# Performance work log

Measured on AMD Instinct MI355X. Metric: run time of the kernel, lower is better.

The kernel has to match this reference:

```python
import jax, jax.numpy as jnp
import numpy as np

MASK_INFTY_APPROX = 1e30
B, L, D = 2, 2048, 1024
H = 16
HD = D // H  # 64
NCODE = 512


def setup_inputs() -> dict:
    key = jax.random.key(0)
    ks = jax.random.split(key, 6)
    s = 1.0 / np.sqrt(D)
    x = jax.random.normal(ks[0], (B, L, D), dtype=jnp.float32)
    Wq = jax.random.normal(ks[1], (D, D), dtype=jnp.float32) * s
    Wk = jax.random.normal(ks[2], (D, D), dtype=jnp.float32) * s
    Wv = jax.random.normal(ks[3], (D, D), dtype=jnp.float32) * s
    Wo = jax.random.normal(ks[4], (D, D), dtype=jnp.float32) * s
    codebook = jax.random.normal(ks[5], (H, NCODE, HD), dtype=jnp.float32)
    return {"x": x, "Wq": Wq, "Wk": Wk, "Wv": Wv, "Wo": Wo, "codebook": codebook}


def _vq(k, codebook):
    # k: [B,H,L,hd], codebook: [H,C,hd]
    dot = jnp.einsum('bhld,hcd->bhlc', k, codebook)
    k2 = jnp.sum(k * k, axis=-1, keepdims=True)            # [B,H,L,1]
    c2 = jnp.sum(codebook * codebook, axis=-1)             # [H,C]
    d2 = k2 - 2.0 * dot + c2[None, :, None, :]             # [B,H,L,C]
    shortcodes = jnp.argmin(d2, axis=-1)                   # [B,H,L]
    h_idx = jnp.arange(H)[None, :, None]
    c_sel = codebook[h_idx, shortcodes]                    # [B,H,L,hd]
    # straight-through quantization
    k_hat = k + jax.lax.stop_gradient(c_sel - k)
    l_commit = jnp.mean(jnp.sum((k - jax.lax.stop_gradient(c_sel)) ** 2, axis=-1))
    l_codebook = jnp.mean(jnp.sum((jax.lax.stop_gradient(k) - c_sel) ** 2, axis=-1))
    return k_hat, shortcodes, l_commit, l_codebook


def reference(x, Wq, Wk, Wv, Wo, codebook):
    q = jnp.einsum('bld,de->ble', x, Wq.T).reshape(B, L, H, HD).transpose(0, 2, 1, 3)
    k = jnp.einsum('bld,de->ble', x, Wk.T).reshape(B, L, H, HD).transpose(0, 2, 1, 3)
    v = jnp.einsum('bld,de->ble', x, Wv.T).reshape(B, L, H, HD).transpose(0, 2, 1, 3)
    k_hat, shortcodes, l_commit, l_codebook = _vq(k, codebook)
    scale = HD ** (-0.5)
    logits = jnp.einsum('bhld,bhtd->bhlt', q, k_hat) * scale  # [B,H,L,L]
    causal_mask = jnp.tril(jnp.ones((L, L), dtype=bool))
    logits = jnp.where(causal_mask[None, None], logits, -MASK_INFTY_APPROX)
    w = jax.nn.softmax(logits, axis=-1)
    attn = jnp.einsum('bhlt,bhtd->bhld', w, v)
    attn = attn.transpose(0, 2, 1, 3).reshape(B, L, D)
    out = jnp.einsum('bld,de->ble', attn, Wo.T)
    return out, l_commit, l_codebook, shortcodes
```

## Files before the change

kernel.cpp:

```cpp
#include <hip/hip_runtime.h>
#include <stdint.h>

#define BB 2
#define HH 16
#define LL 2048
#define DD 1024
#define HDD 64
#define NC 512

typedef __bf16 bf16x8 __attribute__((ext_vector_type(8)));
typedef float f32x4 __attribute__((ext_vector_type(4)));
typedef unsigned short u16x8 __attribute__((ext_vector_type(8)));
typedef unsigned short u16x4 __attribute__((ext_vector_type(4)));

__device__ __forceinline__ unsigned short f2bf(float f) {
  union { float f; unsigned u; } v; v.f = f;
  unsigned u = v.u;
  u += 0x7fffu + ((u >> 16) & 1u);
  return (unsigned short)(u >> 16);
}
__device__ __forceinline__ float bf2f(unsigned short h) {
  union { unsigned u; float f; } v; v.u = ((unsigned)h) << 16;
  return v.f;
}

__device__ __forceinline__ void load_lds16(const unsigned short* g, unsigned short* l) {
  __builtin_amdgcn_global_load_lds((const __attribute__((address_space(1))) void*)g,
                                   (__attribute__((address_space(3))) void*)l, 16, 0, 0);
}

__global__ void cast_all(const float* __restrict__ x, const float* __restrict__ wq,
                         const float* __restrict__ wk, const float* __restrict__ wv,
                         const float* __restrict__ wo, const float* __restrict__ cb,
                         unsigned short* __restrict__ xb, unsigned short* __restrict__ xl,
                         unsigned short* __restrict__ wb, unsigned short* __restrict__ wkl,
                         unsigned short* __restrict__ wob, unsigned short* __restrict__ cbb,
                         unsigned short* __restrict__ cbl, float* __restrict__ lsum) {
  long i = (long)blockIdx.x * blockDim.x + threadIdx.x;
  if (i == 0) lsum[0] = 0.f;
  const long NX4 = 1048576, NW4 = 262144, NCB4 = 131072;
  const long TOT4 = NX4 + 4 * NW4 + NCB4;
  for (long q = i; q < TOT4; q += (long)gridDim.x * blockDim.x) {
    if (q < NX4) {
      long t = q * 4;
      float4 v = *(const float4*)(x + t);
      u16x4 hi, lo;
#pragma unroll
      for (int j = 0; j < 4; j++) {
        float f = ((const float*)&v)[j];
        unsigned short h = f2bf(f);
        hi[j] = h; lo[j] = f2bf(f - bf2f(h));
      }
      *(u16x4*)(xb + t) = hi;
      *(u16x4*)(xl + t) = lo;
    } else if (q < NX4 + NW4) {
      long t = (q - NX4) * 4;
      float4 v = *(const float4*)(wq + t);
      u16x4 hi;
#pragma unroll
      for (int j = 0; j < 4; j++) hi[j] = f2bf(((const float*)&v)[j]);
      *(u16x4*)(wb + t) = hi;
    } else if (q < NX4 + 2 * NW4) {
      long t = (q - NX4 - NW4) * 4;
      float4 v = *(const float4*)(wk + t);
      u16x4 hi, lo;
#pragma unroll
      for (int j = 0; j < 4; j++) {
        float f = ((const float*)&v)[j];
        unsigned short h = f2bf(f);
        hi[j] = h; lo[j] = f2bf(f - bf2f(h));
      }
      *(u16x4*)(wb + 1048576 + t) = hi;
      *(u16x4*)(wkl + t) = lo;
    } else if (q < NX4 + 3 * NW4) {
      long t = (q - NX4 - 2 * NW4) * 4;
      float4 v = *(const float4*)(wv + t);
      u16x4 hi;
#pragma unroll
      for (int j = 0; j < 4; j++) hi[j] = f2bf(((const float*)&v)[j]);
      *(u16x4*)(wb + 2097152 + t) = hi;
    } else if (q < NX4 + 4 * NW4) {
      long t = (q - NX4 - 3 * NW4) * 4;
      float4 v = *(const float4*)(wo + t);
      u16x4 hi;
#pragma unroll
      for (int j = 0; j < 4; j++) hi[j] = f2bf(((const float*)&v)[j]);
      *(u16x4*)(wob + t) = hi;
    } else {
      long t = (q - NX4 - 4 * NW4) * 4;
      float4 v = *(const float4*)(cb + t);
      u16x4 hi, lo;
#pragma unroll
      for (int j = 0; j < 4; j++) {
        float f = ((const float*)&v)[j];
        unsigned short h = f2bf(f);
        hi[j] = h; lo[j] = f2bf(f - bf2f(h));
      }
      *(u16x4*)(cbb + t) = hi;
      *(u16x4*)(cbl + t) = lo;
    }
  }
}

__global__ void c2_kernel(const float* __restrict__ cb, float* __restrict__ c2) {
  int i = blockIdx.x * blockDim.x + threadIdx.x;
  if (i >= HH * NC) return;
  const float* r = cb + (long)i * HDD;
  double s = 0.0;
  for (int j = 0; j < HDD; j++) s += (double)r[j] * (double)r[j];
  c2[i] = (float)s;
}

__global__ __launch_bounds__(256) void gemm_qv(
    const unsigned short* __restrict__ xb, const unsigned short* __restrict__ wb,
    unsigned short* __restrict__ qb, unsigned short* __restrict__ vt) {
  __shared__ __align__(16) unsigned short As[128 * 32];
  __shared__ __align__(16) unsigned short Bs[128 * 32];
  int tid = threadIdx.x;
  int wave = tid >> 6, lane = tid & 63;
  int quad = lane >> 4, col = lane & 15;
  int m0 = blockIdx.y * 128;
  int n0 = blockIdx.x * 128 + (blockIdx.x >= 8 ? 1024 : 0);
  f32x4 acc[4][4] = {};
  int row_in = (wave << 4) + (lane >> 2);
  int seg = lane & 3;
  const unsigned short* gA0 = xb + (long)(m0 + row_in) * DD + seg * 8;
  const unsigned short* gA1 = xb + (long)(m0 + 64 + row_in) * DD + seg * 8;
  const unsigned short* gB0 = wb + (long)(n0 + row_in) * DD + seg * 8;
  const unsigned short* gB1 = wb + (long)(n0 + 64 + row_in) * DD + seg * 8;
  unsigned short* lA0 = As + wave * 512;
  unsigned short* lA1 = As + 2048 + wave * 512;
  unsigned short* lB0 = Bs + wave * 512;
  unsigned short* lB1 = Bs + 2048 + wave * 512;
  int wm = wave & 1, wn = wave >> 1;
  const unsigned short* pa = As + (wm * 64 + col) * 32 + quad * 8;
  const unsigned short* pb = Bs + (wn * 64 + col) * 32 + quad * 8;
  for (int kk = 0; kk < DD; kk += 32) {
    __syncthreads();
    load_lds16(gA0 + kk, lA0);
    load_lds16(gA1 + kk, lA1);
    load_lds16(gB0 + kk, lB0);
    load_lds16(gB1 + kk, lB1);
    __syncthreads();
    bf16x8 af[4], bfr[4];
    for (int t = 0; t < 4; t++) af[t]  = *(const bf16x8*)(pa + t * 512);
    for (int t = 0; t < 4; t++) bfr[t] = *(const bf16x8*)(pb + t * 512);
    for (int mt = 0; mt < 4; mt++)
      for (int nt = 0; nt < 4; nt++)
        acc[mt][nt] = __builtin_amdgcn_mfma_f32_16x16x32_bf16(af[mt], bfr[nt], acc[mt][nt], 0, 0, 0);
  }
  for (int mt = 0; mt < 4; mt++)
    for (int nt = 0; nt < 4; nt++) {
      int mbase = m0 + wm * 64 + mt * 16 + quad * 4;
      int n = n0 + wn * 64 + nt * 16 + col;
      int which = n >> 10, e = n & 1023;
      int h = e >> 6, hd = e & 63;
      for (int r = 0; r < 4; r++) {
        int m = mbase + r;
        int b = m >> 11, l = m & 2047;
        unsigned short val = f2bf(acc[mt][nt][r]);
        long bh = (long)(b * HH + h);
        if (which == 0)      qb[(bh * LL + l) * HDD + hd] = val;
        else                 vt[(bh * HDD + hd) * LL + l] = val;
      }
    }
}

__global__ __launch_bounds__(256) void kvq(
    const unsigned short* __restrict__ xb, const unsigned short* __restrict__ xl,
    const unsigned short* __restrict__ wb, const unsigned short* __restrict__ wkl,
    const float* __restrict__ cb, const float* __restrict__ c2,
    const unsigned short* __restrict__ cbb, const unsigned short* __restrict__ cbl,
    unsigned short* __restrict__ khat, float* __restrict__ scodes,
    float* __restrict__ lsum) {
  __shared__ __align__(16) char smem[53248];
  unsigned short* Ah = (unsigned short*)smem;
  unsigned short* Al = (unsigned short*)(smem + 8192);
  unsigned short* Bh = (unsigned short*)(smem + 16384);
  unsigned short* Bl = (unsigned short*)(smem + 20480);
  float* kfL = (float*)smem;
  unsigned short* CbHb = (unsigned short*)(smem + 34816);
  unsigned short* CbLb = (unsigned short*)(smem + 44032);

  int tid = threadIdx.x;
  int wave = tid >> 6, lane = tid & 63;
  int quad = lane >> 4, col = lane & 15;
  int id = blockIdx.y * 16 + blockIdx.x;
  int xcd = id & 7, sidx = id >> 3;
  int mt4 = xcd * 4 + (sidx >> 4);
  int h = sidx & 15;
  int m0 = mt4 * 128;
  int n0 = h * 64;
  int bgl = m0 >> 11;
  int l0 = m0 & 2047;
  long bh = (long)(bgl * HH + h);
  const float* c2h = c2 + h * NC;

  f32x4 acc[4][2] = {};
  int row_in = (wave << 4) + (lane >> 2);
  int seg = lane & 3;
  const unsigned short* gAh0 = xb + (long)(m0 + row_in) * DD + seg * 8;
  const unsigned short* gAh1 = xb + (long)(m0 + 64 + row_in) * DD + seg * 8;
  const unsigned short* gAl0 = xl + (long)(m0 + row_in) * DD + seg * 8;
  const unsigned short* gAl1 = xl + (long)(m0 + 64 + row_in) * DD + seg * 8;
  const unsigned short* gBh  = wb + (long)(1048576 + (long)(n0 + row_in) * DD) + seg * 8;
  const unsigned short* gBl  = wkl + (long)(n0 + row_in) * DD + seg * 8;
  unsigned short* lAh0 = Ah + wave * 512;
  unsigned short* lAh1 = Ah + 2048 + wave * 512;
  unsigned short* lAl0 = Al + wave * 512;
  unsigned short* lAl1 = Al + 2048 + wave * 512;
  unsigned short* lBh  = Bh + wave * 512;
  unsigned short* lBl  = Bl + wave * 512;
  int wm = wave & 1, wn = wave >> 1;
  const unsigned short* pah = Ah + (wm * 64 + col) * 32 + quad * 8;
  const unsigned short* pal = Al + (wm * 64 + col) * 32 + quad * 8;
  const unsigned short* pbh = Bh + (wn * 32 + col) * 32 + quad * 8;
  const unsigned short* pbl = Bl + (wn * 32 + col) * 32 + quad * 8;
  for (int kk = 0; kk < DD; kk += 32) {
    __syncthreads();
    load_lds16(gAh0 + kk, lAh0);
    load_lds16(gAh1 + kk, lAh1);
    load_lds16(gAl0 + kk, lAl0);
    load_lds16(gAl1 + kk, lAl1);
    load_lds16(gBh + kk, lBh);
    load_lds16(gBl + kk, lBl);
    __syncthreads();
    bf16x8 ah[4], al[4], bhf[2], blf[2];
    for (int t = 0; t < 4; t++) ah[t] = *(const bf16x8*)(pah + t * 512);
    for (int t = 0; t < 4; t++) al[t] = *(const bf16x8*)(pal + t * 512);
    for (int t = 0; t < 2; t++) bhf[t] = *(const bf16x8*)(pbh + t * 512);
    for (int t = 0; t < 2; t++) blf[t] = *(const bf16x8*)(pbl + t * 512);
    for (int mt = 0; mt < 4; mt++)
      for (int nt = 0; nt < 2; nt++) {
        acc[mt][nt] = __builtin_amdgcn_mfma_f32_16x16x32_bf16(ah[mt], bhf[nt], acc[mt][nt], 0, 0, 0);
        acc[mt][nt] = __builtin_amdgcn_mfma_f32_16x16x32_bf16(ah[mt], blf[nt], acc[mt][nt], 0, 0, 0);
        acc[mt][nt] = __builtin_amdgcn_mfma_f32_16x16x32_bf16(al[mt], bhf[nt], acc[mt][nt], 0, 0, 0);
      }
  }
  __syncthreads();
  const unsigned short* cbbh = cbb + (long)h * NC * HDD;
  const unsigned short* cblh = cbl + (long)h * NC * HDD;
  int srow = tid >> 3;
  int sseg = (tid & 7) * 8;
  const unsigned short* gH = cbbh + (long)srow * HDD + sseg;
  const unsigned short* gL = cblh + (long)srow * HDD + sseg;
  int ldsOff = srow * 72 + sseg;
  u16x8 ph0 = *(const u16x8*)(gH);
  u16x8 pl0 = *(const u16x8*)(gL);
  for (int mt = 0; mt < 4; mt++)
    for (int nt = 0; nt < 2; nt++) {
      int rbasew = wm * 64 + mt * 16 + quad * 4;
      int hd = wn * 32 + nt * 16 + col;
      for (int r = 0; r < 4; r++)
        kfL[(rbasew + r) * 68 + hd] = acc[mt][nt][r];
    }
  *(u16x8*)(CbHb + ldsOff) = ph0;
  *(u16x8*)(CbLb + ldsOff) = pl0;
  __syncthreads();

  bf16x8 bfh[2][2], bfl[2][2];
  float k2g[2];
#pragma unroll
  for (int g = 0; g < 2; g++) {
    const float* kp = kfL + (wave * 32 + g * 16 + col) * 68 + quad * 8;
    float4 t0 = *(const float4*)(kp);
    float4 t1 = *(const float4*)(kp + 4);
    float4 t2 = *(const float4*)(kp + 32);
    float4 t3 = *(const float4*)(kp + 36);
    float fv[16];
    fv[0]=t0.x; fv[1]=t0.y; fv[2]=t0.z; fv[3]=t0.w;
    fv[4]=t1.x; fv[5]=t1.y; fv[6]=t1.z; fv[7]=t1.w;
    fv[8]=t2.x; fv[9]=t2.y; fv[10]=t2.z; fv[11]=t2.w;
    fv[12]=t3.x; fv[13]=t3.y; fv[14]=t3.z; fv[15]=t3.w;
    float k2 = 0.f;
#pragma unroll
    for (int j = 0; j < 16; j++) k2 = fmaf(fv[j], fv[j], k2);
    k2 += __shfl_xor(k2, 16);
    k2 += __shfl_xor(k2, 32);
    k2g[g] = k2;
    u16x8 h0, h1, l0u, l1u;
#pragma unroll
    for (int j = 0; j < 8; j++) {
      unsigned short hi = f2bf(fv[j]);
      h0[j] = hi; l0u[j] = f2bf(fv[j] - bf2f(hi));
      unsigned short hi2 = f2bf(fv[8 + j]);
      h1[j] = hi2; l1u[j] = f2bf(fv[8 + j] - bf2f(hi2));
    }
    bfh[g][0] = __builtin_bit_cast(bf16x8, h0);
    bfh[g][1] = __builtin_bit_cast(bf16x8, h1);
    bfl[g][0] = __builtin_bit_cast(bf16x8, l0u);
    bfl[g][1] = __builtin_bit_cast(bf16x8, l1u);
  }
  float b1v[2] = {1e38f, 1e38f}, b2v[2] = {1e38f, 1e38f};
  int b1i[2] = {0x7fffffff, 0x7fffffff}, b2i[2] = {0x7fffffff, 0x7fffffff};
  for (int t = 0; t < 16; t++) {
    int cur = t & 1;
    u16x8 nh, nl;
    if (t < 15) {
      nh = *(const u16x8*)(gH + (t + 1) * 32 * HDD);
      nl = *(const u16x8*)(gL + (t + 1) * 32 * HDD);
    }
    const unsigned short* CbHc = CbHb + cur * 2304;
    const unsigned short* CbLc = CbLb + cur * 2304;
#pragma unroll
    for (int s = 0; s < 2; s++) {
      const unsigned short* rp = CbHc + (s * 16 + col) * 72 + quad * 8;
      const unsigned short* rq = CbLc + (s * 16 + col) * 72 + quad * 8;
      bf16x8 ah0 = *(const bf16x8*)(rp);
      bf16x8 ah1 = *(const bf16x8*)(rp + 32);
      bf16x8 al0 = *(const bf16x8*)(rq);
      bf16x8 al1 = *(const bf16x8*)(rq + 32);
      f32x4 aP0 = {}, aQ0 = {}, aP1 = {}, aQ1 = {};
      aP0 = __builtin_amdgcn_mfma_f32_16x16x32_bf16(ah0, bfh[0][0], aP0, 0, 0, 0);
      aQ0 = __builtin_amdgcn_mfma_f32_16x16x32_bf16(ah1, bfh[0][1], aQ0, 0, 0, 0);
      aP1 = __builtin_amdgcn_mfma_f32_16x16x32_bf16(ah0, bfh[1][0], aP1, 0, 0, 0);
      aQ1 = __builtin_amdgcn_mfma_f32_16x16x32_bf16(ah1, bfh[1][1], aQ1, 0, 0, 0);
      aP0 = __builtin_amdgcn_mfma_f32_16x16x32_bf16(al0, bfh[0][0], aP0, 0, 0, 0);
      aQ0 = __builtin_amdgcn_mfma_f32_16x16x32_bf16(al1, bfh[0][1], aQ0, 0, 0, 0);
      aP1 = __builtin_amdgcn_mfma_f32_16x16x32_bf16(al0, bfh[1][0], aP1, 0, 0, 0);
      aQ1 = __builtin_amdgcn_mfma_f32_16x16x32_bf16(al1, bfh[1][1], aQ1, 0, 0, 0);
      aP0 = __builtin_amdgcn_mfma_f32_16x16x32_bf16(ah0, bfl[0][0], aP0, 0, 0, 0);
      aQ0 = __builtin_amdgcn_mfma_f32_16x16x32_bf16(ah1, bfl[0][1], aQ0, 0, 0, 0);
      aP1 = __builtin_amdgcn_mfma_f32_16x16x32_bf16(ah0, bfl[1][0], aP1, 0, 0, 0);
      aQ1 = __builtin_amdgcn_mfma_f32_16x16x32_bf16(ah1, bfl[1][1], aQ1, 0, 0, 0);
      f32x4 c2v = *(const f32x4*)(c2h + t * 32 + s * 16 + quad * 4);
#pragma unroll
      for (int r = 0; r < 4; r++) {
        int idx = t * 32 + s * 16 + quad * 4 + r;
        float v0 = c2v[r] - 2.0f * (aP0[r] + aQ0[r]);
        if (v0 < b1v[0]) { b2v[0] = b1v[0]; b2i[0] = b1i[0]; b1v[0] = v0; b1i[0] = idx; }
        else if (v0 < b2v[0]) { b2v[0] = v0; b2i[0] = idx; }
        float v1 = c2v[r] - 2.0f * (aP1[r] + aQ1[r]);
        if (v1 < b1v[1]) { b2v[1] = b1v[1]; b2i[1] = b1i[1]; b1v[1] = v1; b1i[1] = idx; }
        else if (v1 < b2v[1]) { b2v[1] = v1; b2i[1] = idx; }
      }
    }
    if (t < 15) {
      *(u16x8*)(CbHb + (cur ^ 1) * 2304 + ldsOff) = nh;
      *(u16x8*)(CbLb + (cur ^ 1) * 2304 + ldsOff) = nl;
    }
    __syncthreads();
  }
  const float DMARG = 0.015625f;
  float partT = 0.f;
  int w0 = 0, w1 = 0;
#pragma unroll
  for (int g = 0; g < 2; g++) {
    float v1 = b1v[g], v2 = b2v[g];
    int i1 = b1i[g], i2 = b2i[g];
#pragma unroll
    for (int d = 16; d <= 32; d <<= 1) {
      float o1v = __shfl_xor(v1, d); int o1i = __shfl_xor(i1, d);
      float o2v = __shfl_xor(v2, d); int o2i = __shfl_xor(i2, d);
      if (o1v < v1 || (o1v == v1 && o1i < i1)) {
        float nv; int ni;
        if (v1 < o2v || (v1 == o2v && i1 < o2i)) { nv = v1; ni = i1; }
        else { nv = o2v; ni = o2i; }
        v1 = o1v; i1 = o1i; v2 = nv; i2 = ni;
      } else {
        if (o1v < v2 || (o1v == v2 && o1i < i2)) { v2 = o1v; i2 = o1i; }
      }
    }
    bool trig = (v2 - v1 <= DMARG);
    float part;
    int widx = i1;
    if (__any(trig)) {
      const float* kpr = kfL + (wave * 32 + g * 16 + col) * 68 + quad * 8;
      float4 f0 = *(const float4*)(kpr);
      float4 f1 = *(const float4*)(kpr + 4);
      float4 f2 = *(const float4*)(kpr + 32);
      float4 f3 = *(const float4*)(kpr + 36);
      const float* c1p = cb + ((long)h * NC + i1) * HDD + quad * 8;
      const float* c2p = cb + ((long)h * NC + i2) * HDD + quad * 8;
      float4 a0 = *(const float4*)(c1p);
      float4 a1 = *(const float4*)(c1p + 4);
      float4 a2 = *(const float4*)(c1p + 32);
      float4 a3 = *(const float4*)(c1p + 36);
      float4 e0 = *(const float4*)(c2p);
      float4 e1 = *(const float4*)(c2p + 4);
      float4 e2 = *(const float4*)(c2p + 32);
      float4 e3 = *(const float4*)(c2p + 36);
      float s1 = 0.f, s2 = 0.f;
#pragma unroll
      for (int j = 0; j < 4; j++) {
        float d;
        d = ((const float*)&f0)[j] - ((const float*)&a0)[j]; s1 = fmaf(d, d, s1);
        d = ((const float*)&f1)[j] - ((const float*)&a1)[j]; s1 = fmaf(d, d, s1);
        d = ((const float*)&f2)[j] - ((const float*)&a2)[j]; s1 = fmaf(d, d, s1);
        d = ((const float*)&f3)[j] - ((const float*)&a3)[j]; s1 = fmaf(d, d, s1);
        d = ((const float*)&f0)[j] - ((const float*)&e0)[j]; s2 = fmaf(d, d, s2);
        d = ((const float*)&f1)[j] - ((const float*)&e1)[j]; s2 = fmaf(d, d, s2);
        d = ((const float*)&f2)[j] - ((const float*)&e2)[j]; s2 = fmaf(d, d, s2);
        d = ((const float*)&f3)[j] - ((const float*)&e3)[j]; s2 = fmaf(d, d, s2);
      }
      s1 += __shfl_xor(s1, 16); s1 += __shfl_xor(s1, 32);
      s2 += __shfl_xor(s2, 16); s2 += __shfl_xor(s2, 32);
      if (trig) {
        if (s2 < s1 || (s2 == s1 && i2 < i1)) { widx = i2; part = s2; }
        else { widx = i1; part = s1; }
      } else {
        part = k2g[g] + v1;
      }
    } else {
      part = k2g[g] + v1;
    }
    if (g == 0) w0 = widx; else w1 = widx;
    if (quad == 0) partT += part;
    if (lane < 16)
      scodes[bh * LL + l0 + wave * 32 + g * 16 + lane] = (float)widx;
  }
  partT += __shfl_xor(partT, 1);  partT += __shfl_xor(partT, 2);
  partT += __shfl_xor(partT, 4);  partT += __shfl_xor(partT, 8);
  partT += __shfl_xor(partT, 16); partT += __shfl_xor(partT, 32);
  if (lane == 0) atomicAdd(lsum, partT);
  {
    int rL = lane >> 1;
    int srcl = rL & 15;
    int c0 = __shfl(w0, srcl);
    int c1 = __shfl(w1, srcl);
    int code = (rL >> 4) ? c1 : c0;
    int p = (lane & 1) * 32;
    const unsigned short* src = cbbh + (long)code * HDD + p;
    unsigned short* dst = khat + (bh * LL + l0 + wave * 32 + rL) * HDD + p;
    *(u16x8*)(dst)      = *(const u16x8*)(src);
    *(u16x8*)(dst + 8)  = *(const u16x8*)(src + 8);
    *(u16x8*)(dst + 16) = *(const u16x8*)(src + 16);
    *(u16x8*)(dst + 24) = *(const u16x8*)(src + 24);
  }
}

__global__ __launch_bounds__(256) void attn_kernel(
    const unsigned short* __restrict__ qb, const unsigned short* __restrict__ khat,
    const unsigned short* __restrict__ vt, unsigned short* __restrict__ attnb) {
  __shared__ __align__(16) unsigned short Pbuf[4][2][16 * 72];
  __shared__ __align__(16) unsigned short Kbuf[64 * 72];
  __shared__ __align__(16) unsigned short Vbuf[64 * 72];
  int tid = threadIdx.x, wave = tid >> 6, lane = tid & 63;
  int quad = lane >> 4, col = lane & 15;
  int id = blockIdx.y * 16 + blockIdx.x;
  int xcd = id & 7, sidx = id >> 3;
  int bh = xcd * 4 + (sidx >> 4);
  int pi = sidx & 15;
  int b = bh >> 4, h = bh & 15;
  int ta = pi, tb = 31 - pi;
  int qbA = ta * 64 + wave * 16;
  int qbB = tb * 64 + wave * 16;
  const unsigned short* qrA = qb + ((long)bh * LL + qbA + col) * HDD;
  const unsigned short* qrB = qb + ((long)bh * LL + qbB + col) * HDD;
  bf16x8 aqA0 = *(const bf16x8*)(qrA + quad * 8);
  bf16x8 aqA1 = *(const bf16x8*)(qrA + 32 + quad * 8);
  bf16x8 aqB0 = *(const bf16x8*)(qrB + quad * 8);
  bf16x8 aqB1 = *(const bf16x8*)(qrB + 32 + quad * 8);
  float lA = 0.f, lB = 0.f;
  f32x4 oA[4] = {}, oB[4] = {};
  unsigned short* PA = Pbuf[wave][0];
  unsigned short* PB = Pbuf[wave][1];
  const unsigned short* kh = khat + (long)bh * LL * HDD;
  const unsigned short* vh = vt + (long)bh * HDD * LL;
  int srow = tid >> 2, sc = (tid & 3) * 8;
  const unsigned short* gK = kh + (long)srow * HDD + sc;
// ... 74 lines not shown
    for (int nt = 0; nt < 4; nt++) {
      const unsigned short* vrow = Vbuf + (nt * 16 + col) * 72;
      bf16x8 v0 = *(const bf16x8*)(vrow + quad * 8);
      bf16x8 v1 = *(const bf16x8*)(vrow + 32 + quad * 8);
      oB[nt] = __builtin_amdgcn_mfma_f32_16x16x32_bf16(apB0, v0, oB[nt], 0, 0, 0);
      oB[nt] = __builtin_amdgcn_mfma_f32_16x16x32_bf16(apB1, v1, oB[nt], 0, 0, 0);
      if (actA) {
        oA[nt] = __builtin_amdgcn_mfma_f32_16x16x32_bf16(apA0, v0, oA[nt], 0, 0, 0);
        oA[nt] = __builtin_amdgcn_mfma_f32_16x16x32_bf16(apA1, v1, oA[nt], 0, 0, 0);
      }
    }
  }
  lA += __shfl_xor(lA, 16); lA += __shfl_xor(lA, 32);
  lB += __shfl_xor(lB, 16); lB += __shfl_xor(lB, 32);
  float invAc = 1.0f / lA;
  float invBc = 1.0f / lB;
  for (int r = 0; r < 4; r++) {
    float invA = __shfl(invAc, quad * 4 + r);
    float invB = __shfl(invBc, quad * 4 + r);
    int rowA = qbA + quad * 4 + r;
    int rowB = qbB + quad * 4 + r;
    for (int nt = 0; nt < 4; nt++) {
      int hd = nt * 16 + col;
      attnb[((long)b * LL + rowA) * DD + h * HDD + hd] = f2bf(oA[nt][r] * invA);
      attnb[((long)b * LL + rowB) * DD + h * HDD + hd] = f2bf(oB[nt][r] * invB);
    }
  }
}

__global__ __launch_bounds__(256) void gemm_out(
    const unsigned short* __restrict__ attnb, const unsigned short* __restrict__ wob,
    float* __restrict__ out) {
  __shared__ __align__(16) unsigned short As[128 * 32];
  __shared__ __align__(16) unsigned short Bs[128 * 32];
  int tid = threadIdx.x;
  int wave = tid >> 6, lane = tid & 63;
  int quad = lane >> 4, col = lane & 15;
  int m0 = blockIdx.y * 128;
  int n0 = blockIdx.x * 128;
  f32x4 acc[4][4] = {};
  int row_in = (wave << 4) + (lane >> 2);
  int seg = lane & 3;
  const unsigned short* gA0 = attnb + (long)(m0 + row_in) * DD + seg * 8;
  const unsigned short* gA1 = attnb + (long)(m0 + 64 + row_in) * DD + seg * 8;
  const unsigned short* gB0 = wob + (long)(n0 + row_in) * DD + seg * 8;
  const unsigned short* gB1 = wob + (long)(n0 + 64 + row_in) * DD + seg * 8;
  unsigned short* lA0 = As + wave * 512;
  unsigned short* lA1 = As + 2048 + wave * 512;
  unsigned short* lB0 = Bs + wave * 512;
  unsigned short* lB1 = Bs + 2048 + wave * 512;
  int wm = wave & 1, wn = wave >> 1;
  const unsigned short* pa = As + (wm * 64 + col) * 32 + quad * 8;
  const unsigned short* pb = Bs + (wn * 64 + col) * 32 + quad * 8;
  for (int kk = 0; kk < DD; kk += 32) {
    __syncthreads();
    load_lds16(gA0 + kk, lA0);
    load_lds16(gA1 + kk, lA1);
    load_lds16(gB0 + kk, lB0);
    load_lds16(gB1 + kk, lB1);
    __syncthreads();
    bf16x8 af[4], bfr[4];
    for (int t = 0; t < 4; t++) af[t]  = *(const bf16x8*)(pa + t * 512);
    for (int t = 0; t < 4; t++) bfr[t] = *(const bf16x8*)(pb + t * 512);
    for (int mt = 0; mt < 4; mt++)
      for (int nt = 0; nt < 4; nt++)
        acc[mt][nt] = __builtin_amdgcn_mfma_f32_16x16x32_bf16(af[mt], bfr[nt], acc[mt][nt], 0, 0, 0);
  }
  for (int mt = 0; mt < 4; mt++)
    for (int nt = 0; nt < 4; nt++) {
      int mbase = m0 + wm * 64 + mt * 16 + quad * 4;
      int n = n0 + wn * 64 + nt * 16 + col;
      for (int r = 0; r < 4; r++)
        out[(long)(mbase + r) * DD + n] = acc[mt][nt][r];
    }
}

__global__ void finalize(const float* __restrict__ lsum, float* __restrict__ out) {
  if (threadIdx.x == 0) {
    float v = lsum[0] / (float)(BB * HH * LL);
    out[4194304] = v;
    out[4194305] = v;
  }
}

extern "C" void kernel_launch(void* const* d_in, const int* in_sizes, int n_in,
                              void* d_out, int out_size, void* d_ws, size_t ws_size,
                              hipStream_t stream) {
  const float* x  = (const float*)d_in[0];
  const float* wq = (const float*)d_in[1];
  const float* wk = (const float*)d_in[2];
  const float* wv = (const float*)d_in[3];
  const float* wo = (const float*)d_in[4];
  const float* cb = (const float*)d_in[5];
  float* out = (float*)d_out;

  char* ws = (char*)d_ws;
  size_t off = 0;
  auto alloc = [&](size_t bytes) {
    void* p = ws + off;
    off = (off + bytes + 255) & ~(size_t)255;
    return p;
  };
  unsigned short* xb    = (unsigned short*)alloc(4194304 * 2);
  unsigned short* xl    = (unsigned short*)alloc(4194304 * 2);
  unsigned short* wb    = (unsigned short*)alloc(3145728 * 2);
  unsigned short* wkl   = (unsigned short*)alloc(1048576 * 2);
  unsigned short* wob   = (unsigned short*)alloc(1048576 * 2);
  unsigned short* cbb   = (unsigned short*)alloc(524288 * 2);
  unsigned short* cbl   = (unsigned short*)alloc(524288 * 2);
  unsigned short* qb    = (unsigned short*)alloc(4194304 * 2);
  unsigned short* vt    = (unsigned short*)alloc(4194304 * 2);
  unsigned short* khat  = (unsigned short*)alloc(4194304 * 2);
  unsigned short* attnb = (unsigned short*)alloc(4194304 * 2);
  float* c2   = (float*)alloc(8192 * 4);
  float* lsum = (float*)alloc(256);

  cast_all<<<dim3(4096), dim3(256), 0, stream>>>(x, wq, wk, wv, wo, cb, xb, xl, wb, wkl, wob, cbb, cbl, lsum);
  c2_kernel<<<dim3(32), dim3(256), 0, stream>>>(cb, c2);
  gemm_qv<<<dim3(16, 32), dim3(256), 0, stream>>>(xb, wb, qb, vt);
  kvq<<<dim3(16, 32), dim3(256), 0, stream>>>(xb, xl, wb, wkl, cb, c2, cbb, cbl, khat, out + 4194306, lsum);
  attn_kernel<<<dim3(16, 32), dim3(256), 0, stream>>>(qb, khat, vt, attnb);
  gemm_out<<<dim3(8, 32), dim3(256), 0, stream>>>(attnb, wob, out);
  finalize<<<dim3(1), dim3(64), 0, stream>>>(lsum, out);
}
```

Measured before the change: 290.6 us.

## Merge QV GEMM and K-VQ into one interleaved launch with smaller tiles

Folds the codebook-norm computation into the cast kernel and merges the Q/V projection GEMM and the K projection plus VQ kernel into one launch. Block indices are interleaved so the two jobs run side by side. The K/VQ tile shrinks from 128 to 64 rows, giving more blocks, and the codebook norms are staged in LDS. The output GEMM N-tile is halved to 64 so it launches twice as many blocks. This cuts launch count and tail idle time and raises occupancy, at the cost of less per-block reuse and possibly uneven block runtimes within the merged grid.

```diff
diff --git a/kernel.cpp b/kernel.cpp
--- a/kernel.cpp
+++ b/kernel.cpp
@@ -35,12 +35,23 @@
                          unsigned short* __restrict__ xb, unsigned short* __restrict__ xl,
                          unsigned short* __restrict__ wb, unsigned short* __restrict__ wkl,
                          unsigned short* __restrict__ wob, unsigned short* __restrict__ cbb,
-                         unsigned short* __restrict__ cbl, float* __restrict__ lsum) {
+                         unsigned short* __restrict__ cbl, float* __restrict__ c2,
+                         float* __restrict__ lsum) {
+  if (blockIdx.x >= 4096) {
+    int i = (blockIdx.x - 4096) * 256 + threadIdx.x;
+    if (i < HH * NC) {
+      const float* r = cb + (long)i * HDD;
+      double s = 0.0;
+      for (int j = 0; j < HDD; j++) s += (double)r[j] * (double)r[j];
+      c2[i] = (float)s;
+    }
+    return;
+  }
   long i = (long)blockIdx.x * blockDim.x + threadIdx.x;
   if (i == 0) lsum[0] = 0.f;
   const long NX4 = 1048576, NW4 = 262144, NCB4 = 131072;
   const long TOT4 = NX4 + 4 * NW4 + NCB4;
-  for (long q = i; q < TOT4; q += (long)gridDim.x * blockDim.x) {
+  for (long q = i; q < TOT4; q += (long)4096 * blockDim.x) {
     if (q < NX4) {
       long t = q * 4;
       float4 v = *(const float4*)(x + t);
@@ -102,135 +113,124 @@
   }
 }
 
-__global__ void c2_kernel(const float* __restrict__ cb, float* __restrict__ c2) {
-  int i = blockIdx.x * blockDim.x + threadIdx.x;
-  if (i >= HH * NC) return;
-  const float* r = cb + (long)i * HDD;
-  double s = 0.0;
-  for (int j = 0; j < HDD; j++) s += (double)r[j] * (double)r[j];
-  c2[i] = (float)s;
-}
-
-__global__ __launch_bounds__(256) void gemm_qv(
-    const unsigned short* __restrict__ xb, const unsigned short* __restrict__ wb,
-    unsigned short* __restrict__ qb, unsigned short* __restrict__ vt) {
-  __shared__ __align__(16) unsigned short As[128 * 32];
-  __shared__ __align__(16) unsigned short Bs[128 * 32];
-  int tid = threadIdx.x;
-  int wave = tid >> 6, lane = tid & 63;
-  int quad = lane >> 4, col = lane & 15;
-  int m0 = blockIdx.y * 128;
-  int n0 = blockIdx.x * 128 + (blockIdx.x >= 8 ? 1024 : 0);
-  f32x4 acc[4][4] = {};
-  int row_in = (wave << 4) + (lane >> 2);
-  int seg = lane & 3;
-  const unsigned short* gA0 = xb + (long)(m0 + row_in) * DD + seg * 8;
-  const unsigned short* gA1 = xb + (long)(m0 + 64 + row_in) * DD + seg * 8;
-  const unsigned short* gB0 = wb + (long)(n0 + row_in) * DD + seg * 8;
-  const unsigned short* gB1 = wb + (long)(n0 + 64 + row_in) * DD + seg * 8;
-  unsigned short* lA0 = As + wave * 512;
-  unsigned short* lA1 = As + 2048 + wave * 512;
-  unsigned short* lB0 = Bs + wave * 512;
-  unsigned short* lB1 = Bs + 2048 + wave * 512;
-  int wm = wave & 1, wn = wave >> 1;
-  const unsigned short* pa = As + (wm * 64 + col) * 32 + quad * 8;
-  const unsigned short* pb = Bs + (wn * 64 + col) * 32 + quad * 8;
-  for (int kk = 0; kk < DD; kk += 32) {
-    __syncthreads();
-    load_lds16(gA0 + kk, lA0);
-    load_lds16(gA1 + kk, lA1);
-    load_lds16(gB0 + kk, lB0);
-    load_lds16(gB1 + kk, lB1);
-    __syncthreads();
-    bf16x8 af[4], bfr[4];
-    for (int t = 0; t < 4; t++) af[t]  = *(const bf16x8*)(pa + t * 512);
-    for (int t = 0; t < 4; t++) bfr[t] = *(const bf16x8*)(pb + t * 512);
-    for (int mt = 0; mt < 4; mt++)
-      for (int nt = 0; nt < 4; nt++)
-        acc[mt][nt] = __builtin_amdgcn_mfma_f32_16x16x32_bf16(af[mt], bfr[nt], acc[mt][nt], 0, 0, 0);
-  }
-  for (int mt = 0; mt < 4; mt++)
-    for (int nt = 0; nt < 4; nt++) {
-      int mbase = m0 + wm * 64 + mt * 16 + quad * 4;
-      int n = n0 + wn * 64 + nt * 16 + col;
-      int which = n >> 10, e = n & 1023;
-      int h = e >> 6, hd = e & 63;
-      for (int r = 0; r < 4; r++) {
-        int m = mbase + r;
-        int b = m >> 11, l = m & 2047;
-        unsigned short val = f2bf(acc[mt][nt][r]);
-        long bh = (long)(b * HH + h);
-        if (which == 0)      qb[(bh * LL + l) * HDD + hd] = val;
-        else                 vt[(bh * HDD + hd) * LL + l] = val;
-      }
-    }
-}
-
-__global__ __launch_bounds__(256) void kvq(
+__global__ __launch_bounds__(256) void qv_kvq(
     const unsigned short* __restrict__ xb, const unsigned short* __restrict__ xl,
     const unsigned short* __restrict__ wb, const unsigned short* __restrict__ wkl,
     const float* __restrict__ cb, const float* __restrict__ c2,
     const unsigned short* __restrict__ cbb, const unsigned short* __restrict__ cbl,
+    unsigned short* __restrict__ qb, unsigned short* __restrict__ vt,
     unsigned short* __restrict__ khat, float* __restrict__ scodes,
     float* __restrict__ lsum) {
-  __shared__ __align__(16) char smem[53248];
-  unsigned short* Ah = (unsigned short*)smem;
-  unsigned short* Al = (unsigned short*)(smem + 8192);
-  unsigned short* Bh = (unsigned short*)(smem + 16384);
-  unsigned short* Bl = (unsigned short*)(smem + 20480);
-  float* kfL = (float*)smem;
-  unsigned short* CbHb = (unsigned short*)(smem + 34816);
-  unsigned short* CbLb = (unsigned short*)(smem + 44032);
-
+  __shared__ __align__(16) char smem[37888];
   int tid = threadIdx.x;
   int wave = tid >> 6, lane = tid & 63;
   int quad = lane >> 4, col = lane & 15;
-  int id = blockIdx.y * 16 + blockIdx.x;
-  int xcd = id & 7, sidx = id >> 3;
-  int mt4 = xcd * 4 + (sidx >> 4);
-  int h = sidx & 15;
-  int m0 = mt4 * 128;
+  int gid = blockIdx.x;
+  int cls = gid % 3;
+
+  if (cls == 2) {
+    unsigned short* As = (unsigned short*)smem;
+    unsigned short* Bs = (unsigned short*)(smem + 8192);
+    int qid = gid / 3;
+    int bx = qid & 15, by = qid >> 4;
+    int m0 = by * 128;
+    int n0 = bx * 128 + (bx >= 8 ? 1024 : 0);
+    f32x4 acc[4][4] = {};
+    int row_in = (wave << 4) + (lane >> 2);
+    int seg = lane & 3;
+    const unsigned short* gA0 = xb + (long)(m0 + row_in) * DD + seg * 8;
+    const unsigned short* gA1 = xb + (long)(m0 + 64 + row_in) * DD + seg * 8;
+    const unsigned short* gB0 = wb + (long)(n0 + row_in) * DD + seg * 8;
+    const unsigned short* gB1 = wb + (long)(n0 + 64 + row_in) * DD + seg * 8;
+    unsigned short* lA0 = As + wave * 512;
+    unsigned short* lA1 = As + 2048 + wave * 512;
+    unsigned short* lB0 = Bs + wave * 512;
+    unsigned short* lB1 = Bs + 2048 + wave * 512;
+    int wm = wave & 1, wn = wave >> 1;
+    const unsigned short* pa = As + (wm * 64 + col) * 32 + quad * 8;
+    const unsigned short* pb = Bs + (wn * 64 + col) * 32 + quad * 8;
+    for (int kk = 0; kk < DD; kk += 32) {
+      __syncthreads();
+      load_lds16(gA0 + kk, lA0);
+      load_lds16(gA1 + kk, lA1);
+      load_lds16(gB0 + kk, lB0);
+      load_lds16(gB1 + kk, lB1);
+      __syncthreads();
+      bf16x8 af[4], bfr[4];
+      for (int t = 0; t < 4; t++) af[t]  = *(const bf16x8*)(pa + t * 512);
+      for (int t = 0; t < 4; t++) bfr[t] = *(const bf16x8*)(pb + t * 512);
+      for (int mt = 0; mt < 4; mt++)
+        for (int nt = 0; nt < 4; nt++)
+          acc[mt][nt] = __builtin_amdgcn_mfma_f32_16x16x32_bf16(af[mt], bfr[nt], acc[mt][nt], 0, 0, 0);
+    }
+    for (int mt = 0; mt < 4; mt++)
+      for (int nt = 0; nt < 4; nt++) {
+        int mbase = m0 + wm * 64 + mt * 16 + quad * 4;
+        int n = n0 + wn * 64 + nt * 16 + col;
+        int which = n >> 10, e = n & 1023;
+        int h = e >> 6, hd = e & 63;
+        for (int r = 0; r < 4; r++) {
+          int m = mbase + r;
+          int b = m >> 11, l = m & 2047;
+          unsigned short val = f2bf(acc[mt][nt][r]);
+          long bh = (long)(b * HH + h);
+          if (which == 0)      qb[(bh * LL + l) * HDD + hd] = val;
+          else                 vt[(bh * HDD + hd) * LL + l] = val;
+        }
+      }
+    return;
+  }
+
+  unsigned short* Ah = (unsigned short*)smem;
+  unsigned short* Al = (unsigned short*)(smem + 4096);
+  unsigned short* Bh = (unsigned short*)(smem + 8192);
+  unsigned short* Bl = (unsigned short*)(smem + 12288);
+  float* kfL = (float*)smem;
+  unsigned short* CbHb = (unsigned short*)(smem + 17408);
+  unsigned short* CbLb = (unsigned short*)(smem + 26624);
+  float* Cs = (float*)(smem + 35840);
+
+  int kid = (gid / 3) * 2 + cls;
+  int mtile = kid & 63;
+  int h = kid >> 6;
+  int m0 = mtile * 64;
   int n0 = h * 64;
   int bgl = m0 >> 11;
   int l0 = m0 & 2047;
   long bh = (long)(bgl * HH + h);
   const float* c2h = c2 + h * NC;
-
-  f32x4 acc[4][2] = {};
+  Cs[tid] = c2h[tid];
+  Cs[tid + 256] = c2h[tid + 256];
+
+  f32x4 acc[2][2] = {};
   int row_in = (wave << 4) + (lane >> 2);
   int seg = lane & 3;
-  const unsigned short* gAh0 = xb + (long)(m0 + row_in) * DD + seg * 8;
-  const unsigned short* gAh1 = xb + (long)(m0 + 64 + row_in) * DD + seg * 8;
-  const unsigned short* gAl0 = xl + (long)(m0 + row_in) * DD + seg * 8;
-  const unsigned short* gAl1 = xl + (long)(m0 + 64 + row_in) * DD + seg * 8;
-  const unsigned short* gBh  = wb + (long)(1048576 + (long)(n0 + row_in) * DD) + seg * 8;
-  const unsigned short* gBl  = wkl + (long)(n0 + row_in) * DD + seg * 8;
-  unsigned short* lAh0 = Ah + wave * 512;
-  unsigned short* lAh1 = Ah + 2048 + wave * 512;
-  unsigned short* lAl0 = Al + wave * 512;
-  unsigned short* lAl1 = Al + 2048 + wave * 512;
-  unsigned short* lBh  = Bh + wave * 512;
-  unsigned short* lBl  = Bl + wave * 512;
+  const unsigned short* gAh = xb + (long)(m0 + row_in) * DD + seg * 8;
+  const unsigned short* gAl = xl + (long)(m0 + row_in) * DD + seg * 8;
+  const unsigned short* gBh = wb + (long)(1048576 + (long)(n0 + row_in) * DD) + seg * 8;
+  const unsigned short* gBl = wkl + (long)(n0 + row_in) * DD + seg * 8;
+  unsigned short* lAh = Ah + wave * 512;
+  unsigned short* lAl = Al + wave * 512;
+  unsigned short* lBh = Bh + wave * 512;
+  unsigned short* lBl = Bl + wave * 512;
   int wm = wave & 1, wn = wave >> 1;
-  const unsigned short* pah = Ah + (wm * 64 + col) * 32 + quad * 8;
-  const unsigned short* pal = Al + (wm * 64 + col) * 32 + quad * 8;
+  const unsigned short* pah = Ah + (wm * 32 + col) * 32 + quad * 8;
+  const unsigned short* pal = Al + (wm * 32 + col) * 32 + quad * 8;
   const unsigned short* pbh = Bh + (wn * 32 + col) * 32 + quad * 8;
   const unsigned short* pbl = Bl + (wn * 32 + col) * 32 + quad * 8;
   for (int kk = 0; kk < DD; kk += 32) {
     __syncthreads();
-    load_lds16(gAh0 + kk, lAh0);
-    load_lds16(gAh1 + kk, lAh1);
-    load_lds16(gAl0 + kk, lAl0);
-    load_lds16(gAl1 + kk, lAl1);
+    load_lds16(gAh + kk, lAh);
+    load_lds16(gAl + kk, lAl);
     load_lds16(gBh + kk, lBh);
     load_lds16(gBl + kk, lBl);
     __syncthreads();
-    bf16x8 ah[4], al[4], bhf[2], blf[2];
-    for (int t = 0; t < 4; t++) ah[t] = *(const bf16x8*)(pah + t * 512);
-    for (int t = 0; t < 4; t++) al[t] = *(const bf16x8*)(pal + t * 512);
+    bf16x8 ah[2], al[2], bhf[2], blf[2];
+    for (int t = 0; t < 2; t++) ah[t] = *(const bf16x8*)(pah + t * 512);
+    for (int t = 0; t < 2; t++) al[t] = *(const bf16x8*)(pal + t * 512);
     for (int t = 0; t < 2; t++) bhf[t] = *(const bf16x8*)(pbh + t * 512);
     for (int t = 0; t < 2; t++) blf[t] = *(const bf16x8*)(pbl + t * 512);
-    for (int mt = 0; mt < 4; mt++)
+    for (int mt = 0; mt < 2; mt++)
       for (int nt = 0; nt < 2; nt++) {
         acc[mt][nt] = __builtin_amdgcn_mfma_f32_16x16x32_bf16(ah[mt], bhf[nt], acc[mt][nt], 0, 0, 0);
         acc[mt][nt] = __builtin_amdgcn_mfma_f32_16x16x32_bf16(ah[mt], blf[nt], acc[mt][nt], 0, 0, 0);
@@ -247,22 +247,21 @@
   int ldsOff = srow * 72 + sseg;
   u16x8 ph0 = *(const u16x8*)(gH);
   u16x8 pl0 = *(const u16x8*)(gL);
-  for (int mt = 0; mt < 4; mt++)
+  for (int mt = 0; mt < 2; mt++)
     for (int nt = 0; nt < 2; nt++) {
-      int rbasew = wm * 64 + mt * 16 + quad * 4;
+      int rw = wm * 32 + mt * 16 + quad * 4;
       int hd = wn * 32 + nt * 16 + col;
       for (int r = 0; r < 4; r++)
-        kfL[(rbasew + r) * 68 + hd] = acc[mt][nt][r];
+        kfL[(rw + r) * 68 + hd] = acc[mt][nt][r];
     }
   *(u16x8*)(CbHb + ldsOff) = ph0;
   *(u16x8*)(CbLb + ldsOff) = pl0;
   __syncthreads();
 
-  bf16x8 bfh[2][2], bfl[2][2];
-  float k2g[2];
-#pragma unroll
-  for (int g = 0; g < 2; g++) {
-    const float* kp = kfL + (wave * 32 + g * 16 + col) * 68 + quad * 8;
+  bf16x8 bh0, bh1, bl0, bl1;
+  float k2;
+  {
+    const float* kp = kfL + (wave * 16 + col) * 68 + quad * 8;
     float4 t0 = *(const float4*)(kp);
     float4 t1 = *(const float4*)(kp + 4);
     float4 t2 = *(const float4*)(kp + 32);
@@ -272,12 +271,11 @@
     fv[4]=t1.x; fv[5]=t1.y; fv[6]=t1.z; fv[7]=t1.w;
     fv[8]=t2.x; fv[9]=t2.y; fv[10]=t2.z; fv[11]=t2.w;
     fv[12]=t3.x; fv[13]=t3.y; fv[14]=t3.z; fv[15]=t3.w;
-    float k2 = 0.f;
+    k2 = 0.f;
 #pragma unroll
     for (int j = 0; j < 16; j++) k2 = fmaf(fv[j], fv[j], k2);
     k2 += __shfl_xor(k2, 16);
     k2 += __shfl_xor(k2, 32);
-    k2g[g] = k2;
     u16x8 h0, h1, l0u, l1u;
 #pragma unroll
     for (int j = 0; j < 8; j++) {
@@ -286,13 +284,13 @@
       unsigned short hi2 = f2bf(fv[8 + j]);
       h1[j] = hi2; l1u[j] = f2bf(fv[8 + j] - bf2f(hi2));
     }
-    bfh[g][0] = __builtin_bit_cast(bf16x8, h0);
-    bfh[g][1] = __builtin_bit_cast(bf16x8, h1);
-    bfl[g][0] = __builtin_bit_cast(bf16x8, l0u);
-    bfl[g][1] = __builtin_bit_cast(bf16x8, l1u);
-  }
-  float b1v[2] = {1e38f, 1e38f}, b2v[2] = {1e38f, 1e38f};
-  int b1i[2] = {0x7fffffff, 0x7fffffff}, b2i[2] = {0x7fffffff, 0x7fffffff};
+    bh0 = __builtin_bit_cast(bf16x8, h0);
+    bh1 = __builtin_bit_cast(bf16x8, h1);
+    bl0 = __builtin_bit_cast(bf16x8, l0u);
+    bl1 = __builtin_bit_cast(bf16x8, l1u);
+  }
+  float b1v = 1e38f, b2v = 1e38f;
+  int b1i = 0x7fffffff, b2i = 0x7fffffff;
   for (int t = 0; t < 16; t++) {
     int cur = t & 1;
     u16x8 nh, nl;
@@ -310,29 +308,20 @@
       bf16x8 ah1 = *(const bf16x8*)(rp + 32);
       bf16x8 al0 = *(const bf16x8*)(rq);
       bf16x8 al1 = *(const bf16x8*)(rq + 32);
-      f32x4 aP0 = {}, aQ0 = {}, aP1 = {}, aQ1 = {};
-      aP0 = __builtin_amdgcn_mfma_f32_16x16x32_bf16(ah0, bfh[0][0], aP0, 0, 0, 0);
-      aQ0 = __builtin_amdgcn_mfma_f32_16x16x32_bf16(ah1, bfh[0][1], aQ0, 0, 0, 0);
-      aP1 = __builtin_amdgcn_mfma_f32_16x16x32_bf16(ah0, bfh[1][0], aP1, 0, 0, 0);
-      aQ1 = __builtin_amdgcn_mfma_f32_16x16x32_bf16(ah1, bfh[1][1], aQ1, 0, 0, 0);
-      aP0 = __builtin_amdgcn_mfma_f32_16x16x32_bf16(al0, bfh[0][0], aP0, 0, 0, 0);
-      aQ0 = __builtin_amdgcn_mfma_f32_16x16x32_bf16(al1, bfh[0][1], aQ0, 0, 0, 0);
-      aP1 = __builtin_amdgcn_mfma_f32_16x16x32_bf16(al0, bfh[1][0], aP1, 0, 0, 0);
-      aQ1 = __builtin_amdgcn_mfma_f32_16x16x32_bf16(al1, bfh[1][1], aQ1, 0, 0, 0);
-      aP0 = __builtin_amdgcn_mfma_f32_16x16x32_bf16(ah0, bfl[0][0], aP0, 0, 0, 0);
-      aQ0 = __builtin_amdgcn_mfma_f32_16x16x32_bf16(ah1, bfl[0][1], aQ0, 0, 0, 0);
-      aP1 = __builtin_amdgcn_mfma_f32_16x16x32_bf16(ah0, bfl[1][0], aP1, 0, 0, 0);
-      aQ1 = __builtin_amdgcn_mfma_f32_16x16x32_bf16(ah1, bfl[1][1], aQ1, 0, 0, 0);
-      f32x4 c2v = *(const f32x4*)(c2h + t * 32 + s * 16 + quad * 4);
+      f32x4 aP = {}, aQ = {};
+      aP = __builtin_amdgcn_mfma_f32_16x16x32_bf16(ah0, bh0, aP, 0, 0, 0);
+      aQ = __builtin_amdgcn_mfma_f32_16x16x32_bf16(ah1, bh1, aQ, 0, 0, 0);
+      aP = __builtin_amdgcn_mfma_f32_16x16x32_bf16(al0, bh0, aP, 0, 0, 0);
+      aQ = __builtin_amdgcn_mfma_f32_16x16x32_bf16(al1, bh1, aQ, 0, 0, 0);
+      aP = __builtin_amdgcn_mfma_f32_16x16x32_bf16(ah0, bl0, aP, 0, 0, 0);
+      aQ = __builtin_amdgcn_mfma_f32_16x16x32_bf16(ah1, bl1, aQ, 0, 0, 0);
+      f32x4 c2v = *(const f32x4*)(Cs + t * 32 + s * 16 + quad * 4);
 #pragma unroll
       for (int r = 0; r < 4; r++) {
+        float val = c2v[r] - 2.0f * (aP[r] + aQ[r]);
         int idx = t * 32 + s * 16 + quad * 4 + r;
-        float v0 = c2v[r] - 2.0f * (aP0[r] + aQ0[r]);
-        if (v0 < b1v[0]) { b2v[0] = b1v[0]; b2i[0] = b1i[0]; b1v[0] = v0; b1i[0] = idx; }
-        else if (v0 < b2v[0]) { b2v[0] = v0; b2i[0] = idx; }
-        float v1 = c2v[r] - 2.0f * (aP1[r] + aQ1[r]);
-        if (v1 < b1v[1]) { b2v[1] = b1v[1]; b2i[1] = b1i[1]; b1v[1] = v1; b1i[1] = idx; }
-        else if (v1 < b2v[1]) { b2v[1] = v1; b2i[1] = idx; }
+        if (val < b1v) { b2v = b1v; b2i = b1i; b1v = val; b1i = idx; }
+        else if (val < b2v) { b2v = val; b2i = idx; }
       }
     }
     if (t < 15) {
@@ -341,91 +330,78 @@
     }
     __syncthreads();
   }
+#pragma unroll
+  for (int d = 16; d <= 32; d <<= 1) {
+    float o1v = __shfl_xor(b1v, d); int o1i = __shfl_xor(b1i, d);
+    float o2v = __shfl_xor(b2v, d); int o2i = __shfl_xor(b2i, d);
+    if (o1v < b1v || (o1v == b1v && o1i < b1i)) {
+      float nv; int ni;
+      if (b1v < o2v || (b1v == o2v && b1i < o2i)) { nv = b1v; ni = b1i; }
+      else { nv = o2v; ni = o2i; }
+      b1v = o1v; b1i = o1i; b2v = nv; b2i = ni;
+    } else {
+      if (o1v < b2v || (o1v == b2v && o1i < b2i)) { b2v = o1v; b2i = o1i; }
+    }
+  }
   const float DMARG = 0.015625f;
-  float partT = 0.f;
-  int w0 = 0, w1 = 0;
-#pragma unroll
-  for (int g = 0; g < 2; g++) {
-    float v1 = b1v[g], v2 = b2v[g];
-    int i1 = b1i[g], i2 = b2i[g];
-#pragma unroll
-    for (int d = 16; d <= 32; d <<= 1) {
-      float o1v = __shfl_xor(v1, d); int o1i = __shfl_xor(i1, d);
-      float o2v = __shfl_xor(v2, d); int o2i = __shfl_xor(i2, d);
-      if (o1v < v1 || (o1v == v1 && o1i < i1)) {
-        float nv; int ni;
-        if (v1 < o2v || (v1 == o2v && i1 < o2i)) { nv = v1; ni = i1; }
-        else { nv = o2v; ni = o2i; }
-        v1 = o1v; i1 = o1i; v2 = nv; i2 = ni;
-      } else {
-        if (o1v < v2 || (o1v == v2 && o1i < i2)) { v2 = o1v; i2 = o1i; }
-      }
-    }
-    bool trig = (v2 - v1 <= DMARG);
-    float part;
-    int widx = i1;
-    if (__any(trig)) {
-      const float* kpr = kfL + (wave * 32 + g * 16 + col) * 68 + quad * 8;
-      float4 f0 = *(const float4*)(kpr);
-      float4 f1 = *(const float4*)(kpr + 4);
-      float4 f2 = *(const float4*)(kpr + 32);
-      float4 f3 = *(const float4*)(kpr + 36);
-      const float* c1p = cb + ((long)h * NC + i1) * HDD + quad * 8;
-      const float* c2p = cb + ((long)h * NC + i2) * HDD + quad * 8;
-      float4 a0 = *(const float4*)(c1p);
-      float4 a1 = *(const float4*)(c1p + 4);
-      float4 a2 = *(const float4*)(c1p + 32);
-      float4 a3 = *(const float4*)(c1p + 36);
-      float4 e0 = *(const float4*)(c2p);
-      float4 e1 = *(const float4*)(c2p + 4);
-      float4 e2 = *(const float4*)(c2p + 32);
-      float4 e3 = *(const float4*)(c2p + 36);
-      float s1 = 0.f, s2 = 0.f;
-#pragma unroll
-      for (int j = 0; j < 4; j++) {
-        float d;
-        d = ((const float*)&f0)[j] - ((const float*)&a0)[j]; s1 = fmaf(d, d, s1);
-        d = ((const float*)&f1)[j] - ((const float*)&a1)[j]; s1 = fmaf(d, d, s1);
-        d = ((const float*)&f2)[j] - ((const float*)&a2)[j]; s1 = fmaf(d, d, s1);
-        d = ((const float*)&f3)[j] - ((const float*)&a3)[j]; s1 = fmaf(d, d, s1);
-        d = ((const float*)&f0)[j] - ((const float*)&e0)[j]; s2 = fmaf(d, d, s2);
-        d = ((const float*)&f1)[j] - ((const float*)&e1)[j]; s2 = fmaf(d, d, s2);
-        d = ((const float*)&f2)[j] - ((const float*)&e2)[j]; s2 = fmaf(d, d, s2);
-        d = ((const float*)&f3)[j] - ((const float*)&e3)[j]; s2 = fmaf(d, d, s2);
-      }
-      s1 += __shfl_xor(s1, 16); s1 += __shfl_xor(s1, 32);
-      s2 += __shfl_xor(s2, 16); s2 += __shfl_xor(s2, 32);
-      if (trig) {
-        if (s2 < s1 || (s2 == s1 && i2 < i1)) { widx = i2; part = s2; }
-        else { widx = i1; part = s1; }
-      } else {
-        part = k2g[g] + v1;
-      }
+  bool trig = (b2v - b1v <= DMARG);
+  float part;
+  int widx = b1i;
+  if (__any(trig)) {
+    const float* kpr = kfL + (wave * 16 + col) * 68 + quad * 8;
+    float4 f0 = *(const float4*)(kpr);
+    float4 f1 = *(const float4*)(kpr + 4);
+    float4 f2 = *(const float4*)(kpr + 32);
+    float4 f3 = *(const float4*)(kpr + 36);
+    const float* c1p = cb + ((long)h * NC + b1i) * HDD + quad * 8;
+    const float* c2p = cb + ((long)h * NC + b2i) * HDD + quad * 8;
+    float4 a0 = *(const float4*)(c1p);
+    float4 a1 = *(const float4*)(c1p + 4);
+    float4 a2 = *(const float4*)(c1p + 32);
+    float4 a3 = *(const float4*)(c1p + 36);
+    float4 e0 = *(const float4*)(c2p);
+    float4 e1 = *(const float4*)(c2p + 4);
+    float4 e2 = *(const float4*)(c2p + 32);
+    float4 e3 = *(const float4*)(c2p + 36);
+    float s1 = 0.f, s2 = 0.f;
+#pragma unroll
+    for (int j = 0; j < 4; j++) {
+      float d;
+      d = ((const float*)&f0)[j] - ((const float*)&a0)[j]; s1 = fmaf(d, d, s1);
+      d = ((const float*)&f1)[j] - ((const float*)&a1)[j]; s1 = fmaf(d, d, s1);
+      d = ((const float*)&f2)[j] - ((const float*)&a2)[j]; s1 = fmaf(d, d, s1);
+      d = ((const float*)&f3)[j] - ((const float*)&a3)[j]; s1 = fmaf(d, d, s1);
+      d = ((const float*)&f0)[j] - ((const float*)&e0)[j]; s2 = fmaf(d, d, s2);
+      d = ((const float*)&f1)[j] - ((const float*)&e1)[j]; s2 = fmaf(d, d, s2);
+      d = ((const float*)&f2)[j] - ((const float*)&e2)[j]; s2 = fmaf(d, d, s2);
+      d = ((const float*)&f3)[j] - ((const float*)&e3)[j]; s2 = fmaf(d, d, s2);
+    }
+    s1 += __shfl_xor(s1, 16); s1 += __shfl_xor(s1, 32);
+    s2 += __shfl_xor(s2, 16); s2 += __shfl_xor(s2, 32);
+    if (trig) {
+      if (s2 < s1 || (s2 == s1 && b2i < b1i)) { widx = b2i; part = s2; }
+      else { widx = b1i; part = s1; }
     } else {
-      part = k2g[g] + v1;
-    }
-    if (g == 0) w0 = widx; else w1 = widx;
-    if (quad == 0) partT += part;
-    if (lane < 16)
-      scodes[bh * LL + l0 + wave * 32 + g * 16 + lane] = (float)widx;
-  }
-  partT += __shfl_xor(partT, 1);  partT += __shfl_xor(partT, 2);
-  partT += __shfl_xor(partT, 4);  partT += __shfl_xor(partT, 8);
-  partT += __shfl_xor(partT, 16); partT += __shfl_xor(partT, 32);
-  if (lane == 0) atomicAdd(lsum, partT);
+      part = k2 + b1v;
+    }
+  } else {
+    part = k2 + b1v;
+  }
+  if (quad != 0) part = 0.f;
+  part += __shfl_xor(part, 1);  part += __shfl_xor(part, 2);
+  part += __shfl_xor(part, 4);  part += __shfl_xor(part, 8);
+  part += __shfl_xor(part, 16); part += __shfl_xor(part, 32);
+  if (lane == 0) atomicAdd(lsum, part);
+  if (lane < 16)
+    scodes[bh * LL + l0 + wave * 16 + lane] = (float)widx;
   {
-    int rL = lane >> 1;
-    int srcl = rL & 15;
-    int c0 = __shfl(w0, srcl);
-    int c1 = __shfl(w1, srcl);
-    int code = (rL >> 4) ? c1 : c0;
-    int p = (lane & 1) * 32;
+    int rL = lane >> 2;
+    int p = (lane & 3) * 16;
+    int code = __shfl(widx, rL);
     const unsigned short* src = cbbh + (long)code * HDD + p;
-    unsigned short* dst = khat + (bh * LL + l0 + wave * 32 + rL) * HDD + p;
-    *(u16x8*)(dst)      = *(const u16x8*)(src);
-    *(u16x8*)(dst + 8)  = *(const u16x8*)(src + 8);
-    *(u16x8*)(dst + 16) = *(const u16x8*)(src + 16);
-    *(u16x8*)(dst + 24) = *(const u16x8*)(src + 24);
+    unsigned short* dst = khat + (bh * LL + l0 + wave * 16 + rL) * HDD + p;
+    *(u16x8*)(dst)     = *(const u16x8*)(src);
+    *(u16x8*)(dst + 8) = *(const u16x8*)(src + 8);
   }
 }
 
@@ -566,44 +542,41 @@
     const unsigned short* __restrict__ attnb, const unsigned short* __restrict__ wob,
     float* __restrict__ out) {
   __shared__ __align__(16) unsigned short As[128 * 32];
-  __shared__ __align__(16) unsigned short Bs[128 * 32];
+  __shared__ __align__(16) unsigned short Bs[64 * 32];
   int tid = threadIdx.x;
   int wave = tid >> 6, lane = tid & 63;
   int quad = lane >> 4, col = lane & 15;
   int m0 = blockIdx.y * 128;
-  int n0 = blockIdx.x * 128;
-  f32x4 acc[4][4] = {};
+  int n0 = blockIdx.x * 64;
+  f32x4 acc[4][2] = {};
   int row_in = (wave << 4) + (lane >> 2);
   int seg = lane & 3;
   const unsigned short* gA0 = attnb + (long)(m0 + row_in) * DD + seg * 8;
   const unsigned short* gA1 = attnb + (long)(m0 + 64 + row_in) * DD + seg * 8;
   const unsigned short* gB0 = wob + (long)(n0 + row_in) * DD + seg * 8;
-  const unsigned short* gB1 = wob + (long)(n0 + 64 + row_in) * DD + seg * 8;
   unsigned short* lA0 = As + wave * 512;
   unsigned short* lA1 = As + 2048 + wave * 512;
   unsigned short* lB0 = Bs + wave * 512;
-  unsigned short* lB1 = Bs + 2048 + wave * 512;
   int wm = wave & 1, wn = wave >> 1;
   const unsigned short* pa = As + (wm * 64 + col) * 32 + quad * 8;
-  const unsigned short* pb = Bs + (wn * 64 + col) * 32 + quad * 8;
+  const unsigned short* pb = Bs + (wn * 32 + col) * 32 + quad * 8;
   for (int kk = 0; kk < DD; kk += 32) {
     __syncthreads();
     load_lds16(gA0 + kk, lA0);
     load_lds16(gA1 + kk, lA1);
     load_lds16(gB0 + kk, lB0);
-    load_lds16(gB1 + kk, lB1);
     __syncthreads();
-    bf16x8 af[4], bfr[4];
+    bf16x8 af[4], bfr[2];
     for (int t = 0; t < 4; t++) af[t]  = *(const bf16x8*)(pa + t * 512);
-    for (int t = 0; t < 4; t++) bfr[t] = *(const bf16x8*)(pb + t * 512);
+    for (int t = 0; t < 2; t++) bfr[t] = *(const bf16x8*)(pb + t * 512);
     for (int mt = 0; mt < 4; mt++)
-      for (int nt = 0; nt < 4; nt++)
+      for (int nt = 0; nt < 2; nt++)
         acc[mt][nt] = __builtin_amdgcn_mfma_f32_16x16x32_bf16(af[mt], bfr[nt], acc[mt][nt], 0, 0, 0);
   }
   for (int mt = 0; mt < 4; mt++)
-    for (int nt = 0; nt < 4; nt++) {
+    for (int nt = 0; nt < 2; nt++) {
       int mbase = m0 + wm * 64 + mt * 16 + quad * 4;
-      int n = n0 + wn * 64 + nt * 16 + col;
+      int n = n0 + wn * 32 + nt * 16 + col;
       for (int r = 0; r < 4; r++)
         out[(long)(mbase + r) * DD + n] = acc[mt][nt][r];
     }
@@ -649,11 +622,9 @@
   float* c2   = (float*)alloc(8192 * 4);
   float* lsum = (float*)alloc(256);
 
-  cast_all<<<dim3(4096), dim3(256), 0, stream>>>(x, wq, wk, wv, wo, cb, xb, xl, wb, wkl, wob, cbb, cbl, lsum);
-  c2_kernel<<<dim3(32), dim3(256), 0, stream>>>(cb, c2);
-  gemm_qv<<<dim3(16, 32), dim3(256), 0, stream>>>(xb, wb, qb, vt);
-  kvq<<<dim3(16, 32), dim3(256), 0, stream>>>(xb, xl, wb, wkl, cb, c2, cbb, cbl, khat, out + 4194306, lsum);
+  cast_all<<<dim3(4128), dim3(256), 0, stream>>>(x, wq, wk, wv, wo, cb, xb, xl, wb, wkl, wob, cbb, cbl, c2, lsum);
+  qv_kvq<<<dim3(1536), dim3(256), 0, stream>>>(xb, xl, wb, wkl, cb, c2, cbb, cbl, qb, vt, khat, out + 4194306, lsum);
   attn_kernel<<<dim3(16, 32), dim3(256), 0, stream>>>(qb, khat, vt, attnb);
-  gemm_out<<<dim3(8, 32), dim3(256), 0, stream>>>(attnb, wob, out);
+  gemm_out<<<dim3(16, 32), dim3(256), 0, stream>>>(attnb, wob, out);
   finalize<<<dim3(1), dim3(64), 0, stream>>>(lsum, out);
 }
```

After: 275.6 us. -5.2%, faster.
